# Performance work log

Measured on AMD Instinct MI355X. Metric: run time of the kernel, lower is better.

## Reference

```python
import jax, jax.numpy as jnp
import numpy as np

N, C, E = 32768, 256, 16
LN_EPS = 1e-5
ENT_EPS = 1e-12


def setup_inputs() -> dict:
    key = jax.random.key(0)
    ks = jax.random.split(key, 8)
    return {
        "inputs": jax.random.normal(ks[0], (N, C), jnp.float32),
        "conv_out": jax.random.normal(ks[1], (N, C), jnp.float32),
        "domain_emb": jax.random.normal(ks[2], (C,), jnp.float32),
        "share_W": jax.random.normal(ks[3], (C, C), jnp.float32) * 0.02,
        "share_b": jnp.zeros((C,), jnp.float32),
        "gate_W": jax.random.normal(ks[4], (C, E), jnp.float32) * 0.1,
        "gate_b": jnp.zeros((E,), jnp.float32),
        "expert_W": jax.random.normal(ks[5], (E, C, C), jnp.float32) * 0.02,
        "expert_b": jnp.zeros((E, C), jnp.float32),
        "ln_gamma": jnp.ones((C,), jnp.float32),
        "ln_beta": jnp.zeros((C,), jnp.float32),
    }


def reference(inputs, conv_out, domain_emb, share_W, share_b, gate_W, gate_b,
              expert_W, expert_b, ln_gamma, ln_beta):
    n_exp = gate_W.shape[-1]

    # shared expert
    share_out = inputs @ share_W + share_b                      # (N, C)

    # LayerNorm on (stand-in) sparse-conv features + domain embedding
    mu = conv_out.mean(-1, keepdims=True)
    var = conv_out.var(-1, keepdims=True)
    route = (conv_out - mu) / jnp.sqrt(var + LN_EPS) * ln_gamma + ln_beta
    route = route + domain_emb                                   # (N, C)

    # router (eval path: no noise)
    gate_logits = route @ gate_W + gate_b                        # (N, E)
    w = jax.nn.softmax(gate_logits.astype(jnp.float32), axis=-1).astype(inputs.dtype)

    # entropy -> dynamic k per token
    entropy = -jnp.sum(w * jnp.log(w + ENT_EPS), axis=-1)        # (N,)
    max_entropy = jnp.log(jnp.float32(n_exp))
    k = jnp.ceil(1.0 + entropy / max_entropy * (n_exp - 1)).astype(jnp.int32)
    k = jnp.clip(k, 1, n_exp)                                    # (N,)

    # dynamic top-k selection mask (sort descending, keep first k)
    order = jnp.argsort(-w, axis=-1)                             # (N, E) descending ranks
    positions = jnp.arange(n_exp)[None, :]
    mask_sorted = positions < k[:, None]                         # (N, E) bool
    inv = jnp.argsort(order, axis=-1)                            # inverse permutation
    sel_mask = jnp.take_along_axis(mask_sorted, inv, axis=-1)    # (N, E) bool, expert-order
    combine = jnp.where(sel_mask, w, jnp.zeros_like(w))          # (N, E) combine weights

    # Switch-style load balancing loss
    frac_tokens = sel_mask.astype(jnp.float32).mean(0)           # (E,)
    frac_probs = w.astype(jnp.float32).mean(0)                   # (E,)
    loss_balance = jnp.mean(frac_tokens * frac_probs) * (n_exp ** 2)

    # expert compute + combine (dense, equivalent to gather/scatter loop)
    expert_out = jnp.einsum('nc,ecd->ned', inputs, expert_W) + expert_b  # (N, E, C)
    moe_out = jnp.einsum('ne,nec->nc', combine, expert_out)     # (N, C)

    return moe_out + share_out, loss_balance
```

## Files before the change

kernel.cpp:

```cpp
#include <hip/hip_runtime.h>
#include <hip/hip_bf16.h>

#define NTOK 32768
#define CH   256
#define NEXP 16

typedef __attribute__((ext_vector_type(8)))  short short8;
typedef __attribute__((ext_vector_type(16))) float f32x16;

#define MFMA32(a, b, c) __builtin_amdgcn_mfma_f32_32x32x16_bf16((a), (b), (c), 0, 0, 0)
#define BC8(v) __builtin_bit_cast(short8, (v))

static __device__ __forceinline__ unsigned short f2bf(float f) {
  unsigned int u = __builtin_bit_cast(unsigned int, f);
  unsigned int r = (u + 0x7fffu + ((u >> 16) & 1u)) >> 16;
  return (unsigned short)r;
}


__global__ __launch_bounds__(256) void wconvert_kernel(
    const float* __restrict__ share_W, const float* __restrict__ expert_W,
    const float* __restrict__ gate_W, uint4* __restrict__ wp,
    float* __restrict__ gwt) {
  if (blockIdx.x == 544) {
    int t = threadIdx.x;
#pragma unroll
    for (int i = 0; i < 16; i++) {
      int idx = i * 256 + t;
      gwt[(idx & 15) * 256 + (idx >> 4)] = gate_W[idx];
    }
    return;
  }
  int g = blockIdx.x * 256 + threadIdx.x;
  int e = g >> 13;
  int r = g & 8191;
  int lane = r & 63;
  int kb = (r >> 6) & 15;
  int db = r >> 10;
  int d  = db * 32 + (lane & 31);
  int k0 = kb * 16 + ((lane >> 5) << 3);
  const float* src = (e < 16) ? (expert_W + (size_t)e * 65536) : share_W;
  unsigned int p[4];
#pragma unroll
  for (int j = 0; j < 4; j++) {
    float f0 = src[(size_t)(k0 + 2 * j) * 256 + d];
    float f1 = src[(size_t)(k0 + 2 * j + 1) * 256 + d];
    p[j] = (unsigned int)f2bf(f0) | ((unsigned int)f2bf(f1) << 16);
  }
  wp[g] = make_uint4(p[0], p[1], p[2], p[3]);
}

__global__ __launch_bounds__(512, 2) void gate_kernel(
    const float* __restrict__ conv_out, const float* __restrict__ domain_emb,
    const float* __restrict__ gwt, const float* __restrict__ gate_b,
    const float* __restrict__ ln_gamma, const float* __restrict__ ln_beta,
    float* __restrict__ combine, float* __restrict__ frac_part) {
  __shared__ float route[8][256];
  __shared__ float fred[2][8][16];
  int t = threadIdx.x, b = blockIdx.x;
  int w = t >> 6, l = t & 63;

  int lc = l * 4;
  float4 g4 = *(const float4*)(ln_gamma + lc);
  float4 be4 = *(const float4*)(ln_beta + lc);
  float4 de4 = *(const float4*)(domain_emb + lc);
  int e = l & 15, q = l >> 4;
  float gb = gate_b[e];

  float4 gwreg[16];
  const float4* gv4 = (const float4*)(gwt + e * 256 + q * 64);
#pragma unroll
  for (int ii = 0; ii < 16; ii++) gwreg[ii] = gv4[ii];

  float psel = 0.f, pw = 0.f;
  int n0 = b * 64 + w * 8;
  float4 x = *(const float4*)(conv_out + (size_t)n0 * 256 + lc);
  for (int i = 0; i < 8; i++) {
    float4 xn = *(const float4*)(conv_out + (size_t)(n0 + ((i + 1) & 7)) * 256 + lc);

    float s1 = x.x + x.y + x.z + x.w;
#pragma unroll
    for (int off = 1; off < 64; off <<= 1) s1 += __shfl_xor(s1, off);
    float mu = s1 * (1.f / 256.f);
    float dx = x.x - mu, dy = x.y - mu, dz = x.z - mu, dw = x.w - mu;
    float s2 = dx * dx + dy * dy + dz * dz + dw * dw;
#pragma unroll
    for (int off = 1; off < 64; off <<= 1) s2 += __shfl_xor(s2, off);
    float rstd = rsqrtf(s2 * (1.f / 256.f) + 1e-5f);
    float4 r;
    r.x = dx * rstd * g4.x + be4.x + de4.x;
    r.y = dy * rstd * g4.y + be4.y + de4.y;
    r.z = dz * rstd * g4.z + be4.z + de4.z;
    r.w = dw * rstd * g4.w + be4.w + de4.w;
    *(float4*)(&route[w][lc]) = r;
    asm volatile("s_waitcnt lgkmcnt(0)" ::: "memory");
    __builtin_amdgcn_wave_barrier();

    float a0 = 0.f, a1 = 0.f, a2 = 0.f, a3 = 0.f;
#pragma unroll
    for (int ii = 0; ii < 16; ii += 4) {
      float4 r0 = *(const float4*)(&route[w][q * 64 + (ii + 0) * 4]);
      float4 r1 = *(const float4*)(&route[w][q * 64 + (ii + 1) * 4]);
      float4 r2 = *(const float4*)(&route[w][q * 64 + (ii + 2) * 4]);
      float4 r3 = *(const float4*)(&route[w][q * 64 + (ii + 3) * 4]);
      a0 += r0.x * gwreg[ii + 0].x + r0.y * gwreg[ii + 0].y + r0.z * gwreg[ii + 0].z + r0.w * gwreg[ii + 0].w;
      a1 += r1.x * gwreg[ii + 1].x + r1.y * gwreg[ii + 1].y + r1.z * gwreg[ii + 1].z + r1.w * gwreg[ii + 1].w;
      a2 += r2.x * gwreg[ii + 2].x + r2.y * gwreg[ii + 2].y + r2.z * gwreg[ii + 2].z + r2.w * gwreg[ii + 2].w;
      a3 += r3.x * gwreg[ii + 3].x + r3.y * gwreg[ii + 3].y + r3.z * gwreg[ii + 3].z + r3.w * gwreg[ii + 3].w;
    }
    float acc = (a0 + a1) + (a2 + a3);
    acc += __shfl_xor(acc, 16);
    acc += __shfl_xor(acc, 32);
    float logit = acc + gb;

    float m = logit;
#pragma unroll
    for (int off = 1; off < 16; off <<= 1) m = fmaxf(m, __shfl_xor(m, off));
    float p = expf(logit - m);
    float sum = p;
#pragma unroll
    for (int off = 1; off < 16; off <<= 1) sum += __shfl_xor(sum, off);
    float wv = p / sum;

    float et = -wv * logf(wv + 1e-12f);
    float ent = et;
#pragma unroll
    for (int off = 1; off < 16; off <<= 1) ent += __shfl_xor(ent, off);
    float kf = ceilf(1.f + ent * (15.f / 2.7725887f));
    int k = (int)kf;
    k = max(1, min(16, k));

    int base = l & 48;
    int rank = 0;
#pragma unroll
    for (int j = 0; j < 16; j++) {
      float wj = __shfl(wv, base + j);
      rank += (wj > wv) || (wj == wv && j < e);
    }
    int sel = rank < k;
    float cmb = sel ? wv : 0.f;
    int n = n0 + i;
    if (l < 16) combine[(size_t)n * 16 + e] = cmb;
    psel += (float)sel;
    pw += wv;

    x = xn;
  }

  if (l < 16) { fred[0][w][l] = psel; fred[1][w][l] = pw; }
  __syncthreads();
  if (t < 32) {
    int kind = t >> 4, ee = t & 15;
    float v = 0.f;
#pragma unroll
    for (int ww = 0; ww < 8; ww++) v += fred[kind][ww][ee];
    frac_part[b * 32 + t] = v;
  }
}

static __device__ __forceinline__ void pref_b(
    uint4 (&breg)[8], const uint4* __restrict__ we, int q) {
#pragma unroll
  for (int f = 0; f < 8; f++) {
    int kbl = f >> 1, d = f & 1;
    breg[f] = we[(size_t)d * 1024 + (q * 4 + kbl) * 64];
  }
}

static __device__ __forceinline__ void slot_mfma(
    f32x16 (&tacc)[2][2], const f32x16& zc, const uint4* __restrict__ at,
    const uint4 (&breg)[8], int q, int abase, int r5, bool first) {
  __builtin_amdgcn_s_setprio(1);
#pragma unroll
  for (int kbl = 0; kbl < 4; kbl++) {
    int kb = q * 4 + kbl;
    int ax = kb * 256 + abase + (r5 ^ kb);
    short8 a0 = BC8(at[ax]);
    short8 a1 = BC8(at[ax + 64]);
    short8 b0 = BC8(breg[kbl * 2 + 0]);
    short8 b1 = BC8(breg[kbl * 2 + 1]);
    if (first && kbl == 0) {
      tacc[0][0] = MFMA32(a0, b0, zc);
      tacc[0][1] = MFMA32(a0, b1, zc);
      tacc[1][0] = MFMA32(a1, b0, zc);
      tacc[1][1] = MFMA32(a1, b1, zc);
    } else {
      tacc[0][0] = MFMA32(a0, b0, tacc[0][0]);
      tacc[0][1] = MFMA32(a0, b1, tacc[0][1]);
      tacc[1][0] = MFMA32(a1, b0, tacc[1][0]);
      tacc[1][1] = MFMA32(a1, b1, tacc[1][1]);
    }
  }
  __builtin_amdgcn_s_setprio(0);
}

__global__ __launch_bounds__(512, 2) void moe_gemm_kernel(
    const float* __restrict__ inputs, const uint4* __restrict__ wpack,
    const float* __restrict__ combine, const float* __restrict__ expert_b,
    const float* __restrict__ share_b, float* __restrict__ out) {
  extern __shared__ __align__(16) char smem[];
  uint4* at    = (uint4*)smem;
  float* wtile = (float*)(smem + 65536);

  int t = threadIdx.x, b = blockIdx.x;
  int w = t >> 6, l = t & 63;
  int mbp = w >> 2;
  int dbp = w & 3;
  int r5 = l & 31, hi = l >> 5;

#pragma unroll
  for (int i = 0; i < 8; i++) {
    int idx = i * 512 + t;
    int row = idx >> 5;
    int j = idx & 31;
    const float4* src = (const float4*)(inputs + ((size_t)b * 128 + row) * 256 + j * 8);
    float4 f0 = src[0], f1 = src[1];
    unsigned int p0 = (unsigned int)f2bf(f0.x) | ((unsigned int)f2bf(f0.y) << 16);
    unsigned int p1 = (unsigned int)f2bf(f0.z) | ((unsigned int)f2bf(f0.w) << 16);
    unsigned int p2 = (unsigned int)f2bf(f1.x) | ((unsigned int)f2bf(f1.y) << 16);
    unsigned int p3 = (unsigned int)f2bf(f1.z) | ((unsigned int)f2bf(f1.w) << 16);
    int kb = j >> 1, hib = j & 1;
    at[kb * 256 + (row >> 5) * 64 + hib * 32 + ((row & 31) ^ kb)] =
        make_uint4(p0, p1, p2, p3);
  }
  {
    const float* cg = combine + (size_t)b * 2048;
#pragma unroll
    for (int i = 0; i < 4; i++) {
      int idx = i * 512 + t;
      wtile[(idx & 15) * 128 + (idx >> 4)] = cg[idx];
    }
  }

  const uint4* wb = wpack + (size_t)(dbp * 2) * 1024 + l;
  uint4 bregA[8], bregB[8];
  pref_b(bregA, wb, 0);

  __syncthreads();

  f32x16 facc[2][2];
#pragma unroll
  for (int mi = 0; mi < 2; mi++)
#pragma unroll
    for (int d = 0; d < 2; d++)
#pragma unroll
      for (int r = 0; r < 16; r++) facc[mi][d][r] = 0.f;
  f32x16 zc;
#pragma unroll
  for (int r = 0; r < 16; r++) zc[r] = 0.f;

  f32x16 tacc[2][2];
  int rowoff = hi * 4;
  int abase = mbp * 128 + hi * 32;

  for (int e = 0; e < 17; e++) {
    const uint4* we = wb + (size_t)e * 8192;
    pref_b(bregB, we, 1);
    slot_mfma(tacc, zc, at, bregA, 0, abase, r5, true);
    pref_b(bregA, we, 2);
    slot_mfma(tacc, zc, at, bregB, 1, abase, r5, false);
    pref_b(bregB, we, 3);
    slot_mfma(tacc, zc, at, bregA, 2, abase, r5, false);
    if (e < 16) pref_b(bregA, we + 8192, 0);
    slot_mfma(tacc, zc, at, bregB, 3, abase, r5, false);

    if (e < 16) {
#pragma unroll
      for (int mi = 0; mi < 2; mi++)
#pragma unroll
        for (int rg = 0; rg < 4; rg++) {
          float4 w4 = *(const float4*)&wtile[e * 128 + (mbp * 2 + mi) * 32 + 8 * rg + rowoff];
          float wj[4] = {w4.x, w4.y, w4.z, w4.w};
#pragma unroll
          for (int j = 0; j < 4; j++) {
            facc[mi][0][rg * 4 + j] += wj[j] * tacc[mi][0][rg * 4 + j];
            facc[mi][1][rg * 4 + j] += wj[j] * tacc[mi][1][rg * 4 + j];
          }
        }
    } else {
#pragma unroll
      for (int mi = 0; mi < 2; mi++)
#pragma unroll
        for (int r = 0; r < 16; r++) {
          facc[mi][0][r] += tacc[mi][0][r];
          facc[mi][1][r] += tacc[mi][1][r];
        }
    }
  }

  int col = r5;
  int cg0 = (dbp * 2 + 0) * 32 + col;
  int cg1 = (dbp * 2 + 1) * 32 + col;
  float sb0 = share_b[cg0], sb1 = share_b[cg1];
  float eb0[16], eb1[16];
#pragma unroll
  for (int e2 = 0; e2 < 16; e2++) {
    eb0[e2] = expert_b[e2 * 256 + cg0];
    eb1[e2] = expert_b[e2 * 256 + cg1];
  }
#pragma unroll
  for (int e2 = 0; e2 < 16; e2++)
#pragma unroll
    for (int mi = 0; mi < 2; mi++)
#pragma unroll
      for (int rg = 0; rg < 4; rg++) {
        float4 w4 = *(const float4*)&wtile[e2 * 128 + (mbp * 2 + mi) * 32 + 8 * rg + rowoff];
        float wj[4] = {w4.x, w4.y, w4.z, w4.w};
#pragma unroll
        for (int j = 0; j < 4; j++) {
          facc[mi][0][rg * 4 + j] += wj[j] * eb0[e2];
          facc[mi][1][rg * 4 + j] += wj[j] * eb1[e2];
        }
      }
#pragma unroll
  for (int mi = 0; mi < 2; mi++)
#pragma unroll
    for (int r = 0; r < 16; r++) {
      int row = (mbp * 2 + mi) * 32 + (r & 3) + ((r >> 2) << 3) + rowoff;
      size_t n = (size_t)b * 128 + row;
      out[n * 256 + cg0] = facc[mi][0][r] + sb0;
      out[n * 256 + cg1] = facc[mi][1][r] + sb1;
    }
}

__global__ __launch_bounds__(256) void finalize_kernel(
    const float* __restrict__ frac_part, float* __restrict__ loss_out) {
  __shared__ float acc[8][32];
  int t = threadIdx.x;
  int col = t & 31, seg = t >> 5;
  float s = 0.f;
  for (int i = seg; i < 512; i += 8) s += frac_part[i * 32 + col];
  acc[seg][col] = s;
  __syncthreads();
  if (t < 32) {
    float v = 0.f;
#pragma unroll
    for (int sg = 0; sg < 8; sg++) v += acc[sg][t];
    acc[0][t] = v;
  }
  __syncthreads();
  if (t == 0) {
    float loss = 0.f;
    for (int e = 0; e < 16; e++) {
      float ft = acc[0][e] * (1.f / 32768.f);
      float fp = acc[0][16 + e] * (1.f / 32768.f);
      loss += ft * fp;
    }
    loss_out[0] = loss * 16.f;
  }
}

extern "C" void kernel_launch(void* const* d_in, const int* in_sizes, int n_in,
                              void* d_out, int out_size, void* d_ws, size_t ws_size,
                              hipStream_t stream) {
  const float* inputs   = (const float*)d_in[0];
  const float* conv_out = (const float*)d_in[1];
  const float* demb     = (const float*)d_in[2];
  const float* share_W  = (const float*)d_in[3];
  const float* share_b  = (const float*)d_in[4];
  const float* gate_W   = (const float*)d_in[5];
  const float* gate_b   = (const float*)d_in[6];
  const float* expert_W = (const float*)d_in[7];
  const float* expert_b = (const float*)d_in[8];
  const float* ln_g     = (const float*)d_in[9];
  const float* ln_b     = (const float*)d_in[10];
  float* out = (float*)d_out;
  char* ws = (char*)d_ws;

  uint4* wpack   = (uint4*)(ws);
  float* gwt     = (float*)(ws + 2228224);
  float* combine = (float*)(ws + 2244608);
  float* frac    = (float*)(ws + 4341760);

  hipFuncSetAttribute((const void*)moe_gemm_kernel,
                      hipFuncAttributeMaxDynamicSharedMemorySize, 73728);

  wconvert_kernel<<<dim3(545), dim3(256), 0, stream>>>(share_W, expert_W, gate_W,
                                                       wpack, gwt);
  gate_kernel<<<dim3(512), dim3(512), 0, stream>>>(conv_out, demb, gwt, gate_b,
                                                   ln_g, ln_b, combine, frac);
  moe_gemm_kernel<<<dim3(256), dim3(512), 73728, stream>>>(inputs, wpack, combine,
                                                           expert_b, share_b, out);
  finalize_kernel<<<dim3(1), dim3(256), 0, stream>>>(frac, out + 8388608);
}
```

Measured before the change: 241.2 us.

## Merge prep kernels, fold finalize into GEMM, deepen B-prefetch pipeline to three buffers

Weight conversion and gating are merged into one prep kernel. Gate weights are now transposed in shared memory per block instead of in a separate global pass. The loss finalize becomes an extra block of the GEMM kernel, so the launch count drops from four to two. The GEMM loop is flattened into 68 slots with triple-buffered register prefetch of B fragments two slots ahead, which raises register pressure in exchange for more latency hiding.

```diff
diff --git a/kernel.cpp b/kernel.cpp
--- a/kernel.cpp
+++ b/kernel.cpp
@@ -18,47 +18,47 @@
 }
 
 
-__global__ __launch_bounds__(256) void wconvert_kernel(
+__global__ __launch_bounds__(512, 2) void prep_kernel(
+    const float* __restrict__ conv_out, const float* __restrict__ domain_emb,
+    const float* __restrict__ gate_W, const float* __restrict__ gate_b,
+    const float* __restrict__ ln_gamma, const float* __restrict__ ln_beta,
     const float* __restrict__ share_W, const float* __restrict__ expert_W,
-    const float* __restrict__ gate_W, uint4* __restrict__ wp,
-    float* __restrict__ gwt) {
-  if (blockIdx.x == 544) {
-    int t = threadIdx.x;
-#pragma unroll
-    for (int i = 0; i < 16; i++) {
-      int idx = i * 256 + t;
-      gwt[(idx & 15) * 256 + (idx >> 4)] = gate_W[idx];
-    }
+    float* __restrict__ combine, float* __restrict__ frac_part,
+    uint4* __restrict__ wp) {
+  int t = threadIdx.x, b = blockIdx.x;
+
+  if (b >= 512) {
+    int g = (b - 512) * 512 + t;
+    int e = g >> 13;
+    int r = g & 8191;
+    int lane = r & 63;
+    int kb = (r >> 6) & 15;
+    int db = r >> 10;
+    int d  = db * 32 + (lane & 31);
+    int k0 = kb * 16 + ((lane >> 5) << 3);
+    const float* src = (e < 16) ? (expert_W + (size_t)e * 65536) : share_W;
+    unsigned int p[4];
+#pragma unroll
+    for (int j = 0; j < 4; j++) {
+      float f0 = src[(size_t)(k0 + 2 * j) * 256 + d];
+      float f1 = src[(size_t)(k0 + 2 * j + 1) * 256 + d];
+      p[j] = (unsigned int)f2bf(f0) | ((unsigned int)f2bf(f1) << 16);
+    }
+    wp[g] = make_uint4(p[0], p[1], p[2], p[3]);
     return;
   }
-  int g = blockIdx.x * 256 + threadIdx.x;
-  int e = g >> 13;
-  int r = g & 8191;
-  int lane = r & 63;
-  int kb = (r >> 6) & 15;
-  int db = r >> 10;
-  int d  = db * 32 + (lane & 31);
-  int k0 = kb * 16 + ((lane >> 5) << 3);
-  const float* src = (e < 16) ? (expert_W + (size_t)e * 65536) : share_W;
-  unsigned int p[4];
-#pragma unroll
-  for (int j = 0; j < 4; j++) {
-    float f0 = src[(size_t)(k0 + 2 * j) * 256 + d];
-    float f1 = src[(size_t)(k0 + 2 * j + 1) * 256 + d];
-    p[j] = (unsigned int)f2bf(f0) | ((unsigned int)f2bf(f1) << 16);
-  }
-  wp[g] = make_uint4(p[0], p[1], p[2], p[3]);
-}
-
-__global__ __launch_bounds__(512, 2) void gate_kernel(
-    const float* __restrict__ conv_out, const float* __restrict__ domain_emb,
-    const float* __restrict__ gwt, const float* __restrict__ gate_b,
-    const float* __restrict__ ln_gamma, const float* __restrict__ ln_beta,
-    float* __restrict__ combine, float* __restrict__ frac_part) {
+
   __shared__ float route[8][256];
+  __shared__ __align__(16) float gwT[16 * 260];
   __shared__ float fred[2][8][16];
-  int t = threadIdx.x, b = blockIdx.x;
   int w = t >> 6, l = t & 63;
+
+#pragma unroll
+  for (int i = 0; i < 8; i++) {
+    int idx = i * 512 + t;
+    gwT[(idx & 15) * 260 + (idx >> 4)] = gate_W[idx];
+  }
+  __syncthreads();
 
   int lc = l * 4;
   float4 g4 = *(const float4*)(ln_gamma + lc);
@@ -68,9 +68,9 @@
   float gb = gate_b[e];
 
   float4 gwreg[16];
-  const float4* gv4 = (const float4*)(gwt + e * 256 + q * 64);
-#pragma unroll
-  for (int ii = 0; ii < 16; ii++) gwreg[ii] = gv4[ii];
+#pragma unroll
+  for (int ii = 0; ii < 16; ii++)
+    gwreg[ii] = *(const float4*)&gwT[e * 260 + q * 64 + ii * 4];
 
   float psel = 0.f, pw = 0.f;
   int n0 = b * 64 + w * 8;
@@ -159,17 +159,29 @@
 }
 
 static __device__ __forceinline__ void pref_b(
-    uint4 (&breg)[8], const uint4* __restrict__ we, int q) {
+    uint4 (&breg)[8], const uint4* __restrict__ wb, int s) {
+  int en = s >> 2, qn = s & 3;
+  const uint4* we = wb + (size_t)en * 8192;
 #pragma unroll
   for (int f = 0; f < 8; f++) {
     int kbl = f >> 1, d = f & 1;
-    breg[f] = we[(size_t)d * 1024 + (q * 4 + kbl) * 64];
-  }
-}
-
-static __device__ __forceinline__ void slot_mfma(
-    f32x16 (&tacc)[2][2], const f32x16& zc, const uint4* __restrict__ at,
-    const uint4 (&breg)[8], int q, int abase, int r5, bool first) {
+    breg[f] = we[(size_t)d * 1024 + (qn * 4 + kbl) * 64];
+  }
+}
+
+static __device__ __forceinline__ void do_slot(
+    f32x16 (&facc)[2][2], f32x16 (&tacc)[2][2], const uint4* __restrict__ at,
+    const uint4 (&breg)[8], int s, int abase, int r5,
+    const float* __restrict__ wtile, int mbp, int rowoff) {
+  int q = s & 3;
+  if (q == 0) {
+#pragma unroll
+    for (int mi = 0; mi < 2; mi++)
+#pragma unroll
+      for (int d = 0; d < 2; d++)
+#pragma unroll
+        for (int r = 0; r < 16; r++) tacc[mi][d][r] = 0.f;
+  }
   __builtin_amdgcn_s_setprio(1);
 #pragma unroll
   for (int kbl = 0; kbl < 4; kbl++) {
@@ -179,30 +191,76 @@
     short8 a1 = BC8(at[ax + 64]);
     short8 b0 = BC8(breg[kbl * 2 + 0]);
     short8 b1 = BC8(breg[kbl * 2 + 1]);
-    if (first && kbl == 0) {
-      tacc[0][0] = MFMA32(a0, b0, zc);
-      tacc[0][1] = MFMA32(a0, b1, zc);
-      tacc[1][0] = MFMA32(a1, b0, zc);
-      tacc[1][1] = MFMA32(a1, b1, zc);
+    tacc[0][0] = MFMA32(a0, b0, tacc[0][0]);
+    tacc[0][1] = MFMA32(a0, b1, tacc[0][1]);
+    tacc[1][0] = MFMA32(a1, b0, tacc[1][0]);
+    tacc[1][1] = MFMA32(a1, b1, tacc[1][1]);
+  }
+  __builtin_amdgcn_s_setprio(0);
+  if (q == 3) {
+    int e = s >> 2;
+    if (e < 16) {
+#pragma unroll
+      for (int mi = 0; mi < 2; mi++)
+#pragma unroll
+        for (int rg = 0; rg < 4; rg++) {
+          float4 w4 = *(const float4*)&wtile[e * 128 + (mbp * 2 + mi) * 32 + 8 * rg + rowoff];
+          float wj[4] = {w4.x, w4.y, w4.z, w4.w};
+#pragma unroll
+          for (int j = 0; j < 4; j++) {
+            facc[mi][0][rg * 4 + j] += wj[j] * tacc[mi][0][rg * 4 + j];
+            facc[mi][1][rg * 4 + j] += wj[j] * tacc[mi][1][rg * 4 + j];
+          }
+        }
     } else {
-      tacc[0][0] = MFMA32(a0, b0, tacc[0][0]);
-      tacc[0][1] = MFMA32(a0, b1, tacc[0][1]);
-      tacc[1][0] = MFMA32(a1, b0, tacc[1][0]);
-      tacc[1][1] = MFMA32(a1, b1, tacc[1][1]);
-    }
-  }
-  __builtin_amdgcn_s_setprio(0);
+#pragma unroll
+      for (int mi = 0; mi < 2; mi++)
+#pragma unroll
+        for (int r = 0; r < 16; r++) {
+          facc[mi][0][r] += tacc[mi][0][r];
+          facc[mi][1][r] += tacc[mi][1][r];
+        }
+    }
+  }
 }
 
 __global__ __launch_bounds__(512, 2) void moe_gemm_kernel(
     const float* __restrict__ inputs, const uint4* __restrict__ wpack,
     const float* __restrict__ combine, const float* __restrict__ expert_b,
-    const float* __restrict__ share_b, float* __restrict__ out) {
+    const float* __restrict__ share_b, float* __restrict__ out,
+    const float* __restrict__ frac_part) {
   extern __shared__ __align__(16) char smem[];
+  int t = threadIdx.x, b = blockIdx.x;
+
+  if (b == 256) {
+    float* acc = (float*)smem;
+    int col = t & 31, seg = t >> 5;
+    float s = 0.f;
+    for (int i = seg; i < 512; i += 16) s += frac_part[i * 32 + col];
+    acc[seg * 32 + col] = s;
+    __syncthreads();
+    if (t < 32) {
+      float v = 0.f;
+#pragma unroll
+      for (int sg = 0; sg < 16; sg++) v += acc[sg * 32 + t];
+      acc[t] = v;
+    }
+    __syncthreads();
+    if (t == 0) {
+      float loss = 0.f;
+      for (int e = 0; e < 16; e++) {
+        float ft = acc[e] * (1.f / 32768.f);
+        float fp = acc[16 + e] * (1.f / 32768.f);
+        loss += ft * fp;
+      }
+      out[8388608] = loss * 16.f;
+    }
+    return;
+  }
+
   uint4* at    = (uint4*)smem;
   float* wtile = (float*)(smem + 65536);
 
-  int t = threadIdx.x, b = blockIdx.x;
   int w = t >> 6, l = t & 63;
   int mbp = w >> 2;
   int dbp = w & 3;
@@ -233,8 +291,9 @@
   }
 
   const uint4* wb = wpack + (size_t)(dbp * 2) * 1024 + l;
-  uint4 bregA[8], bregB[8];
-  pref_b(bregA, wb, 0);
+  uint4 bA[8], bB[8], bC[8];
+  pref_b(bA, wb, 0);
+  pref_b(bB, wb, 1);
 
   __syncthreads();
 
@@ -245,46 +304,26 @@
     for (int d = 0; d < 2; d++)
 #pragma unroll
       for (int r = 0; r < 16; r++) facc[mi][d][r] = 0.f;
-  f32x16 zc;
-#pragma unroll
-  for (int r = 0; r < 16; r++) zc[r] = 0.f;
-
   f32x16 tacc[2][2];
+
   int rowoff = hi * 4;
   int abase = mbp * 128 + hi * 32;
 
-  for (int e = 0; e < 17; e++) {
-    const uint4* we = wb + (size_t)e * 8192;
-    pref_b(bregB, we, 1);
-    slot_mfma(tacc, zc, at, bregA, 0, abase, r5, true);
-    pref_b(bregA, we, 2);
-    slot_mfma(tacc, zc, at, bregB, 1, abase, r5, false);
-    pref_b(bregB, we, 3);
-    slot_mfma(tacc, zc, at, bregA, 2, abase, r5, false);
-    if (e < 16) pref_b(bregA, we + 8192, 0);
-    slot_mfma(tacc, zc, at, bregB, 3, abase, r5, false);
-
-    if (e < 16) {
-#pragma unroll
-      for (int mi = 0; mi < 2; mi++)
-#pragma unroll
-        for (int rg = 0; rg < 4; rg++) {
-          float4 w4 = *(const float4*)&wtile[e * 128 + (mbp * 2 + mi) * 32 + 8 * rg + rowoff];
-          float wj[4] = {w4.x, w4.y, w4.z, w4.w};
-#pragma unroll
-          for (int j = 0; j < 4; j++) {
-            facc[mi][0][rg * 4 + j] += wj[j] * tacc[mi][0][rg * 4 + j];
-            facc[mi][1][rg * 4 + j] += wj[j] * tacc[mi][1][rg * 4 + j];
-          }
-        }
-    } else {
-#pragma unroll
-      for (int mi = 0; mi < 2; mi++)
-#pragma unroll
-        for (int r = 0; r < 16; r++) {
-          facc[mi][0][r] += tacc[mi][0][r];
-          facc[mi][1][r] += tacc[mi][1][r];
-        }
+  for (int s0 = 0; s0 < 68; s0 += 3) {
+    {
+      int s = s0;
+      if (s + 2 < 68) pref_b(bC, wb, s + 2);
+      do_slot(facc, tacc, at, bA, s, abase, r5, wtile, mbp, rowoff);
+    }
+    if (s0 + 1 < 68) {
+      int s = s0 + 1;
+      if (s + 2 < 68) pref_b(bA, wb, s + 2);
+      do_slot(facc, tacc, at, bB, s, abase, r5, wtile, mbp, rowoff);
+    }
+    if (s0 + 2 < 68) {
+      int s = s0 + 2;
+      if (s + 2 < 68) pref_b(bB, wb, s + 2);
+      do_slot(facc, tacc, at, bC, s, abase, r5, wtile, mbp, rowoff);
     }
   }
 
@@ -321,33 +360,6 @@
       out[n * 256 + cg0] = facc[mi][0][r] + sb0;
       out[n * 256 + cg1] = facc[mi][1][r] + sb1;
     }
-}
-
-__global__ __launch_bounds__(256) void finalize_kernel(
-    const float* __restrict__ frac_part, float* __restrict__ loss_out) {
-  __shared__ float acc[8][32];
-  int t = threadIdx.x;
-  int col = t & 31, seg = t >> 5;
-  float s = 0.f;
-  for (int i = seg; i < 512; i += 8) s += frac_part[i * 32 + col];
-  acc[seg][col] = s;
-  __syncthreads();
-  if (t < 32) {
-    float v = 0.f;
-#pragma unroll
-    for (int sg = 0; sg < 8; sg++) v += acc[sg][t];
-    acc[0][t] = v;
-  }
-  __syncthreads();
-  if (t == 0) {
-    float loss = 0.f;
-    for (int e = 0; e < 16; e++) {
-      float ft = acc[0][e] * (1.f / 32768.f);
-      float fp = acc[0][16 + e] * (1.f / 32768.f);
-      loss += ft * fp;
-    }
-    loss_out[0] = loss * 16.f;
-  }
 }
 
 extern "C" void kernel_launch(void* const* d_in, const int* in_sizes, int n_in,
@@ -368,18 +380,15 @@
   char* ws = (char*)d_ws;
 
   uint4* wpack   = (uint4*)(ws);
-  float* gwt     = (float*)(ws + 2228224);
-  float* combine = (float*)(ws + 2244608);
-  float* frac    = (float*)(ws + 4341760);
+  float* combine = (float*)(ws + 2228224);
+  float* frac    = (float*)(ws + 4325376);
 
   hipFuncSetAttribute((const void*)moe_gemm_kernel,
                       hipFuncAttributeMaxDynamicSharedMemorySize, 73728);
 
-  wconvert_kernel<<<dim3(545), dim3(256), 0, stream>>>(share_W, expert_W, gate_W,
-                                                       wpack, gwt);
-  gate_kernel<<<dim3(512), dim3(512), 0, stream>>>(conv_out, demb, gwt, gate_b,
-                                                   ln_g, ln_b, combine, frac);
-  moe_gemm_kernel<<<dim3(256), dim3(512), 73728, stream>>>(inputs, wpack, combine,
-                                                           expert_b, share_b, out);
-  finalize_kernel<<<dim3(1), dim3(256), 0, stream>>>(frac, out + 8388608);
-}
+  prep_kernel<<<dim3(784), dim3(512), 0, stream>>>(
+      conv_out, demb, gate_W, gate_b, ln_g, ln_b, share_W, expert_W,
+      combine, frac, wpack);
+  moe_gemm_kernel<<<dim3(257), dim3(512), 73728, stream>>>(
+      inputs, wpack, combine, expert_b, share_b, out, frac);
+}
```

Result: slower. 305.9 us (+26.8%).
